# Kernel tuning notes

Hardware: AMD Instinct MI355X
Metric: run time of the kernel (lower is better)

## Reference

```python
import jax, jax.numpy as jnp
import numpy as np

N_HEAD, D_HEAD, D_MODEL = 16, 64, 1024
QLEN, MEMLEN, BSZ = 1024, 1024, 2
KLEN = QLEN + MEMLEN  # rlen == klen
LN_EPS = 1e-5
NEG = -1e30


def _rel_shift(x):
    # x: [qlen, rlen, bsz, n_head] -> Transformer-XL relative shift
    q, r, b, n = x.shape
    zp = jnp.zeros((q, 1, b, n), x.dtype)
    xp = jnp.concatenate([zp, x], axis=1).reshape(r + 1, q, b, n)
    return xp[1:].reshape(q, r, b, n)


def _layer_norm(x, gamma, beta):
    mu = jnp.mean(x, axis=-1, keepdims=True)
    var = jnp.mean((x - mu) ** 2, axis=-1, keepdims=True)
    return (x - mu) * jax.lax.rsqrt(var + LN_EPS) * gamma + beta


def setup_inputs() -> dict:
    key = jax.random.key(0)
    ks = jax.random.split(key, 8)
    w = jax.random.normal(ks[0], (QLEN, BSZ, D_MODEL), jnp.float32)
    r = jax.random.normal(ks[1], (KLEN, D_MODEL), jnp.float32)
    r_w_bias = jax.random.normal(ks[2], (N_HEAD, D_HEAD), jnp.float32) * 0.02
    r_r_bias = jax.random.normal(ks[3], (N_HEAD, D_HEAD), jnp.float32) * 0.02
    mems = jax.random.normal(ks[4], (MEMLEN, BSZ, D_MODEL), jnp.float32)
    W_qkv = jax.random.normal(ks[5], (D_MODEL, 3 * N_HEAD * D_HEAD), jnp.float32) * 0.02
    W_r = jax.random.normal(ks[6], (D_MODEL, N_HEAD * D_HEAD), jnp.float32) * 0.02
    W_o = jax.random.normal(ks[7], (N_HEAD * D_HEAD, D_MODEL), jnp.float32) * 0.02
    ln_gamma = jnp.ones((D_MODEL,), jnp.float32)
    ln_beta = jnp.zeros((D_MODEL,), jnp.float32)
    # causal mask with memory: key j visible to query i iff j <= i + MEMLEN (True = keep)
    attn_mask = jnp.arange(KLEN)[None, :] <= (jnp.arange(QLEN)[:, None] + MEMLEN)
    return {"w": w, "r": r, "r_w_bias": r_w_bias, "r_r_bias": r_r_bias,
            "mems": mems, "attn_mask": attn_mask, "W_qkv": W_qkv, "W_r": W_r,
            "W_o": W_o, "ln_gamma": ln_gamma, "ln_beta": ln_beta}


def reference(w, r, r_w_bias, r_r_bias, mems, attn_mask, W_qkv, W_r, W_o, ln_gamma, ln_beta):
    qlen, bsz = w.shape[0], w.shape[1]
    scale = 1.0 / (D_HEAD ** 0.5)
    cat = jnp.concatenate([mems, w], axis=0)            # [klen, b, d_model]
    klen = cat.shape[0]
    w_heads = cat @ W_qkv                                # [klen, b, 3*H*D]
    r_head_k = (r @ W_r).reshape(-1, N_HEAD, D_HEAD)     # [rlen, H, D]
    w_head_q, w_head_k, w_head_v = jnp.split(w_heads, 3, axis=-1)
    w_head_q = w_head_q[-qlen:].reshape(qlen, bsz, N_HEAD, D_HEAD)
    w_head_k = w_head_k.reshape(klen, bsz, N_HEAD, D_HEAD)
    w_head_v = w_head_v.reshape(klen, bsz, N_HEAD, D_HEAD)
    AC = jnp.einsum('ibnd,jbnd->ijbn', w_head_q + r_w_bias, w_head_k)
    BD = jnp.einsum('ibnd,jnd->ijbn', w_head_q + r_r_bias, r_head_k)
    BD = _rel_shift(BD)
    attn_score = (AC + BD) * scale                       # [q, k, b, n]
    attn_score = jnp.where(attn_mask[:, :, None, None], attn_score, NEG)
    attn_prob = jax.nn.softmax(attn_score, axis=1)
    attn_vec = jnp.einsum('ijbn,jbnd->ibnd', attn_prob, w_head_v)
    attn_vec = attn_vec.reshape(qlen, bsz, N_HEAD * D_HEAD)
    attn_out = attn_vec @ W_o                            # [q, b, d_model]
    return _layer_norm(w + attn_out, ln_gamma, ln_beta)
```

## Files before the change

### kernel.cpp

```cpp
#include <hip/hip_runtime.h>
#include <hip/hip_bf16.h>

#define NHEAD 16
#define DHEAD 64
#define DMODEL 1024
#define QLEN 1024
#define MEMLEN 1024
#define BSZ 2
#define KLEN 2048
#define LN_EPS 1e-5f

typedef __hip_bfloat16 bf16;
typedef __attribute__((ext_vector_type(8))) short short8;
typedef __attribute__((ext_vector_type(4))) float f32x4;

__device__ __forceinline__ float b2f(bf16 x) { return __bfloat162float(x); }
__device__ __forceinline__ bf16 f2b(float x) { return __float2bfloat16(x); }
__device__ __forceinline__ short f2bs(float f) {
    bf16 h = __float2bfloat16(f);
    return *reinterpret_cast<short*>(&h);
}
__device__ __forceinline__ float s2f(short s) {
    bf16 h = *reinterpret_cast<bf16*>(&s);
    return __bfloat162float(h);
}

#define MFMA16(a, b, c) __builtin_amdgcn_mfma_f32_16x16x32_bf16(a, b, c, 0, 0, 0)

#define AS1 __attribute__((address_space(1)))
#define AS3 __attribute__((address_space(3)))
__device__ __forceinline__ void gld16(const bf16* g, bf16* l) {
    __builtin_amdgcn_global_load_lds((const AS1 void*)(uintptr_t)g,
                                     (AS3 void*)(uint32_t)(uintptr_t)l, 16, 0, 0);
}

__global__ __launch_bounds__(256)
void prep(const float* __restrict__ mems, const float* __restrict__ w,
          const float* __restrict__ r, const float* __restrict__ Wqkv,
          const float* __restrict__ Wr, const float* __restrict__ Wo,
          bf16* __restrict__ Abf, bf16* __restrict__ rbf,
          bf16* __restrict__ Wqkvt, bf16* __restrict__ Wrt,
          bf16* __restrict__ Wot) {
    __shared__ bf16 T[64][65];
    const int id = blockIdx.x;
    const int t = threadIdx.x;
    if (id < 6144) {
        const float* src;
        bf16* dst;
        int off;
        if (id < 2048)      { src = mems; dst = Abf;                       off = id; }
        else if (id < 4096) { src = w;    dst = Abf + (size_t)2048 * 1024; off = id - 2048; }
        else                { src = r;    dst = rbf;                       off = id - 4096; }
        int i = off * 256 + t;
        const float4 v = reinterpret_cast<const float4*>(src)[i];
        bf16 o[4] = {f2b(v.x), f2b(v.y), f2b(v.z), f2b(v.w)};
        reinterpret_cast<ulong1*>(dst)[i] = *reinterpret_cast<ulong1*>(o);
        return;
    }
    int tid2 = id - 6144;
    const float* in;
    bf16* out;
    int N, tn, tile;
    if (tid2 < 768)       { in = Wqkv; out = Wqkvt; N = 3072; tn = 48; tile = tid2; }
    else if (tid2 < 1024) { in = Wr;   out = Wrt;   N = 1024; tn = 16; tile = tid2 - 768; }
    else                  { in = Wo;   out = Wot;   N = 1024; tn = 16; tile = tid2 - 1024; }
    const int K = 1024;
    const int n0 = (tile % tn) * 64, k0 = (tile / tn) * 64;
    #pragma unroll
    for (int e = 0; e < 16; e++) {
        int flat = e * 256 + t;
        int kl = flat >> 6, nl = flat & 63;
        T[kl][nl] = f2b(in[(size_t)(k0 + kl) * N + n0 + nl]);
    }
    __syncthreads();
    #pragma unroll
    for (int e = 0; e < 16; e++) {
        int flat = e * 256 + t;
        int nl = flat >> 6, kl = flat & 63;
        out[(size_t)(n0 + nl) * K + k0 + kl] = T[kl][nl];
    }
}

__global__ __launch_bounds__(256)
void gemm_mfma(const bf16* __restrict__ A, const bf16* __restrict__ Bt,
               const bf16* __restrict__ A2, const bf16* __restrict__ B2,
               int M, int N, int K, int mode,
               const float* __restrict__ rwb, const float* __restrict__ rrb,
               bf16* __restrict__ Qw, bf16* __restrict__ Qr,
               bf16* __restrict__ Kb, bf16* __restrict__ Vt,
               bf16* __restrict__ Cb, float* __restrict__ Cf) {
    const int bm = blockIdx.x * 128, bn = blockIdx.y * 128;
    int sub = 0;
    const bf16* Ap = A;
    const bf16* Bp = Bt;
    if (mode == 0 && bm < 2048 && bn < 1024) { sub = 1; Ap = A2; Bp = B2; }
    __shared__ bf16 As[128 * 32];
    __shared__ bf16 Bs[128 * 32];
    const int t = threadIdx.x;
    const int w = t >> 6, lane = t & 63, quad = lane >> 4, l16 = lane & 15;
    const int wm = (w >> 1) * 64, wn = (w & 1) * 64;
    const int lrow = lane >> 2, lcol = (lane & 3) * 8;

    f32x4 acc[4][4];
    #pragma unroll
    for (int mt = 0; mt < 4; mt++)
        #pragma unroll
        for (int nt = 0; nt < 4; nt++) acc[mt][nt] = (f32x4){0.f, 0.f, 0.f, 0.f};

    for (int k0 = 0; k0 < K; k0 += 32) {
        #pragma unroll
        for (int e = 0; e < 2; e++) {
            int ch = w + 4 * e;
            int row = ch * 16 + lrow;
            gld16(Ap + (size_t)(bm + row) * K + k0 + lcol, As + ch * 512);
            gld16(Bp + (size_t)(bn + row) * K + k0 + lcol, Bs + ch * 512);
        }
        __syncthreads();
        short8 af[4], bfr[4];
        #pragma unroll
        for (int mt = 0; mt < 4; mt++)
            af[mt] = *reinterpret_cast<short8*>(&As[(wm + 16 * mt + l16) * 32 + quad * 8]);
        #pragma unroll
        for (int nt = 0; nt < 4; nt++)
            bfr[nt] = *reinterpret_cast<short8*>(&Bs[(wn + 16 * nt + l16) * 32 + quad * 8]);
        #pragma unroll
        for (int mt = 0; mt < 4; mt++)
            #pragma unroll
            for (int nt = 0; nt < 4; nt++)
                acc[mt][nt] = MFMA16(af[mt], bfr[nt], acc[mt][nt]);
        __syncthreads();
    }

    #pragma unroll
    for (int mt = 0; mt < 4; mt++)
        #pragma unroll
        for (int nt = 0; nt < 4; nt++)
            #pragma unroll
            for (int r = 0; r < 4; r++) {
                int m = bm + wm + 16 * mt + quad * 4 + r;
                int c = bn + wn + 16 * nt + l16;
                float v = acc[mt][nt][r];
                if (sub) {
                    Cb[(size_t)m * 1024 + c] = f2b(v);
                } else if (mode == 0) {
                    int seg = c >> 10, cc = c & 1023;
                    if (seg == 0) {
                        if (m >= 2048) {
                            size_t o = (size_t)(m - 2048) * 1024 + cc;
                            Qw[o] = f2b(v + rwb[cc]);
                            Qr[o] = f2b(v + rrb[cc]);
                        }
                    } else if (seg == 1) {
                        Kb[(size_t)m * 1024 + cc] = f2b(v);
                    } else {
                        Vt[((size_t)cc * 2 + (m & 1)) * 2048 + (m >> 1)] = f2b(v);
                    }
                } else {
                    Cf[(size_t)m * N + c] = v;
                }
            }
}

__global__ __launch_bounds__(256, 3)
void attn_mfma(const bf16* __restrict__ Qw, const bf16* __restrict__ Qr,
               const bf16* __restrict__ Kb, const bf16* __restrict__ Vt,
               const bf16* __restrict__ Rk, float* __restrict__ Opart0,
               float* __restrict__ Opart1, float2* __restrict__ ML) {
    const int id = blockIdx.x;
    const int xcd = id & 7, local = id >> 3;
    const int quarter = local >> 5, idx = local & 31;
    const int a = idx >> 1, p = idx & 1;
    int i0, pidx, half;
    if (quarter < 2) { i0 = a;      pidx = p;     half = quarter; }
    else             { i0 = 15 - a; pidx = 2 + p; half = quarter - 2; }
    const int pair = xcd * 4 + pidx;
    const int b = pair & 1, n = pair >> 1;
    const int I0 = i0 * 64;
    const int T = i0 + 17;
    const int h0 = (T + 1) >> 1;
    const int t_beg = half ? h0 : 0;
    const int t_end = half ? T : h0;

    const int tid = threadIdx.x;
    const int w = tid >> 6, lane = tid & 63;
    const int quad = lane >> 4, l16 = lane & 15;
    const int qbase = I0 + 16 * w;
    const int ln8 = lane >> 3;
    const int cs = (lane & 7) ^ (ln8 & 7);
    const int q0 = (quad ^ (l16 & 7)) * 8;
    const int q1 = q0 ^ 32;

    __shared__ bf16 Ks[64 * 64];
    __shared__ bf16 Vs[64 * 64];
    __shared__ bf16 Rs[2][64 * 64];
    __shared__ short WlB_s[4][16 * 80];
    __shared__ short Pb_s[4][16 * 72];
    short* WlB = WlB_s[w];
    short* Pb = Pb_s[w];

    short8 aqw[2], aqr[2];
    {
        const bf16* qp = Qw + ((size_t)(qbase + l16) * 2 + b) * 1024 + n * 64 + quad * 8;
        aqw[0] = *reinterpret_cast<const short8*>(qp);
        aqw[1] = *reinterpret_cast<const short8*>(qp + 32);
        const bf16* qp2 = Qr + ((size_t)(qbase + l16) * 2 + b) * 1024 + n * 64 + quad * 8;
        aqr[0] = *reinterpret_cast<const short8*>(qp2);
        aqr[1] = *reinterpret_cast<const short8*>(qp2 + 32);
    }

    f32x4 O[4];
    #pragma unroll
    for (int d = 0; d < 4; d++) O[d] = (f32x4){0.f, 0.f, 0.f, 0.f};
    float m_run = -1e30f;
    float pl[4] = {0.f, 0.f, 0.f, 0.f};

    const int koff = b * 1024 + n * 64 + cs * 8;
    const size_t voff = (size_t)n * 262144 + b * 2048 + cs * 8;
    const int rcol = n * 64 + cs * 8;
    const int rbl = 48 - 16 * w;
    const int RB = 960 - I0;

    auto stageKV = [&](int tt) {
        const int J0 = tt * 64;
        #pragma unroll
        for (int e = 0; e < 2; e++) {
            int ch = w + 4 * e;
            int krow = J0 + ch * 8 + ln8;
            gld16(Kb + (size_t)krow * 2048 + koff, Ks + ch * 512);
            int dl = ch * 8 + ln8;
            gld16(Vt + (size_t)dl * 4096 + voff + J0, Vs + ch * 512);
        }
    };
    auto stageR = [&](int u) {
        bf16* rd = Rs[u & 1];
        #pragma unroll
        for (int e = 0; e < 2; e++) {
            int ch = w + 4 * e;
            int rrow = min(RB + u * 64 + ch * 8 + ln8, 2047);
            gld16(Rk + (size_t)rrow * 1024 + rcol, rd + ch * 512);
        }
    };

    stageR(t_beg);

    for (int tt = t_beg; tt < t_end; tt++) {
        stageKV(tt);
        stageR(tt + 1);
        __syncthreads();

        const bf16* R0 = Rs[tt & 1];
        const bf16* R1 = Rs[(tt + 1) & 1];
        const int J0 = tt * 64;

        #pragma unroll
        for (int s = 0; s < 5; s++) {
            int rb2 = rbl + 16 * s;
            const bf16* Rb = (rb2 & 64) ? R1 : R0;
            int rh = (rb2 & 63) + l16;
            short8 b0 = *reinterpret_cast<const short8*>(&Rb[rh * 64 + q0]);
            short8 b1 = *reinterpret_cast<const short8*>(&Rb[rh * 64 + q1]);
            f32x4 acc = (f32x4){0.f, 0.f, 0.f, 0.f};
            __builtin_amdgcn_s_setprio(1);
            acc = MFMA16(aqr[0], b0, acc);
            acc = MFMA16(aqr[1], b1, acc);
            __builtin_amdgcn_s_setprio(0);
            #pragma unroll
            for (int r = 0; r < 4; r++)
                WlB[(quad * 4 + r) * 80 + 16 * s + l16] = f2bs(acc[r]);
        }

        float sv[4][4];
        #pragma unroll
        for (int n16 = 0; n16 < 4; n16++) {
            int kr = 16 * n16 + l16;
            short8 k0 = *reinterpret_cast<const short8*>(&Ks[kr * 64 + q0]);
            short8 k1 = *reinterpret_cast<const short8*>(&Ks[kr * 64 + q1]);
            f32x4 acc = (f32x4){0.f, 0.f, 0.f, 0.f};
            __builtin_amdgcn_s_setprio(1);
            acc = MFMA16(aqw[0], k0, acc);
            acc = MFMA16(aqw[1], k1, acc);
            __builtin_amdgcn_s_setprio(0);
            #pragma unroll
            for (int r = 0; r < 4; r++) {
                int row = quad * 4 + r, col = 16 * n16 + l16;
                float s = (acc[r] + s2f(WlB[row * 80 + col - row + 15])) * 0.125f;
                if (J0 + col > qbase + row + MEMLEN) s = -1e30f;
                sv[n16][r] = s;
            }
        }

        float mx = sv[0][0];
        #pragma unroll
        for (int n16 = 0; n16 < 4; n16++)
            #pragma unroll
            for (int r = 0; r < 4; r++) mx = fmaxf(mx, sv[n16][r]);
        #pragma unroll
        for (int msk = 1; msk < 16; msk <<= 1) mx = fmaxf(mx, __shfl_xor(mx, msk));
        if (mx > m_run + 8.f) {
            const float alpha = __expf(m_run - mx);
            m_run = mx;
            #pragma unroll
            for (int r = 0; r < 4; r++) pl[r] *= alpha;
            #pragma unroll
            for (int d = 0; d < 4; d++)
                #pragma unroll
                for (int r = 0; r < 4; r++) O[d][r] *= alpha;
        }
        #pragma unroll
        for (int n16 = 0; n16 < 4; n16++)
            #pragma unroll
            for (int r = 0; r < 4; r++) sv[n16][r] = __expf(sv[n16][r] - m_run);
        #pragma unroll
        for (int r = 0; r < 4; r++)
            pl[r] += sv[0][r] + sv[1][r] + sv[2][r] + sv[3][r];

        #pragma unroll
        for (int n16 = 0; n16 < 4; n16++)
            #pragma unroll
            for (int r = 0; r < 4; r++)
                Pb[(quad * 4 + r) * 72 + 16 * n16 + l16] = f2bs(sv[n16][r]);
        short8 ap0 = *reinterpret_cast<short8*>(&Pb[l16 * 72 + quad * 8]);
        short8 ap1 = *reinterpret_cast<short8*>(&Pb[l16 * 72 + 32 + quad * 8]);

        __builtin_amdgcn_s_setprio(1);
        #pragma unroll
        for (int ds = 0; ds < 4; ds++) {
            int dr = 16 * ds + l16;
            short8 v0 = *reinterpret_cast<const short8*>(&Vs[dr * 64 + q0]);
            short8 v1 = *reinterpret_cast<const short8*>(&Vs[dr * 64 + q1]);
            O[ds] = MFMA16(ap0, v0, O[ds]);
            O[ds] = MFMA16(ap1, v1, O[ds]);
        }
        __builtin_amdgcn_s_setprio(0);

        __syncthreads();
    }

    float lr[4];
    #pragma unroll
    for (int r = 0; r < 4; r++) {
        float s = pl[r];
        #pragma unroll
        for (int msk = 1; msk < 16; msk <<= 1) s += __shfl_xor(s, msk);
        lr[r] = s;
    }
    if (l16 == 0) {
        #pragma unroll
        for (int r = 0; r < 4; r++) {
            int q = qbase + quad * 4 + r;
            ML[(size_t)half * 32768 + (q * 2 + b) * 16 + n] =
                make_float2(m_run, lr[r]);
        }
    }
    float* Od = half ? Opart1 : Opart0;
    #pragma unroll
    for (int ds = 0; ds < 4; ds++)
        #pragma unroll
        for (int r = 0; r < 4; r++) {
            int q = qbase + quad * 4 + r;
            Od[((size_t)q * 2 + b) * 1024 + n * 64 + 16 * ds + l16] =
                O[ds][r] / lr[r];
        }
}

__global__ __launch_bounds__(256)
void attn_combine(const float* __restrict__ O0, const float* __restrict__ O1,
                  const float2* __restrict__ ML, bf16* __restrict__ AVbf) {
    const int row = blockIdx.x;
    const int t = threadIdx.x;
    const int n = t >> 4;
    const float2 a0 = ML[row * 16 + n];
    const float2 a1 = ML[32768 + row * 16 + n];
    const float m = fmaxf(a0.x, a1.x);
    float w0 = a0.y * __expf(a0.x - m);
    float w1 = a1.y * __expf(a1.x - m);
    const float inv = 1.f / (w0 + w1);
    w0 *= inv; w1 *= inv;
    const f32x4 p0 = reinterpret_cast<const f32x4*>(O0)[row * 256 + t];
    const f32x4 p1 = reinterpret_cast<const f32x4*>(O1)[row * 256 + t];
    short o[4];
    #pragma unroll
    for (int j = 0; j < 4; j++) o[j] = f2bs(p0[j] * w0 + p1[j] * w1);
    reinterpret_cast<ulong1*>(AVbf)[row * 256 + t] = *reinterpret_cast<ulong1*>(o);
}

__global__ __launch_bounds__(256)
void ln_res(const float* __restrict__ ao, const float* __restrict__ w,
            const float* __restrict__ gamma, const float* __restrict__ beta,
            float* __restrict__ out) {
    const int m = blockIdx.x;
    const int t = threadIdx.x;
    __shared__ float red[256];
    float x[4];
    #pragma unroll
    for (int e = 0; e < 4; e++) {
        int c = e * 256 + t;
        x[e] = ao[(size_t)m * DMODEL + c] + w[(size_t)m * DMODEL + c];
    }
    float s = x[0] + x[1] + x[2] + x[3];
    red[t] = s;
    __syncthreads();
    #pragma unroll
    for (int off = 128; off; off >>= 1) {
        if (t < off) red[t] += red[t + off];
        __syncthreads();
    }
    const float mu = red[0] * (1.f / 1024.f);
    __syncthreads();
    float s2 = 0.f;
    #pragma unroll
    for (int e = 0; e < 4; e++) { float dx = x[e] - mu; s2 += dx * dx; }
    red[t] = s2;
    __syncthreads();
    #pragma unroll
    for (int off = 128; off; off >>= 1) {
        if (t < off) red[t] += red[t + off];
        __syncthreads();
    }
    const float rstd = rsqrtf(red[0] * (1.f / 1024.f) + LN_EPS);
    #pragma unroll
    for (int e = 0; e < 4; e++) {
        int c = e * 256 + t;
        out[(size_t)m * DMODEL + c] = (x[e] - mu) * rstd * gamma[c] + beta[c];
    }
}

extern "C" void kernel_launch(void* const* d_in, const int* in_sizes, int n_in,
                              void* d_out, int out_size, void* d_ws, size_t ws_size,
                              hipStream_t stream) {
    const float* w        = (const float*)d_in[0];
    const float* r        = (const float*)d_in[1];
    const float* r_w_bias = (const float*)d_in[2];
    const float* r_r_bias = (const float*)d_in[3];
    const float* mems     = (const float*)d_in[4];
    const float* W_qkv    = (const float*)d_in[6];
    const float* W_r      = (const float*)d_in[7];
    const float* W_o      = (const float*)d_in[8];
    const float* gamma    = (const float*)d_in[9];
    const float* beta     = (const float*)d_in[10];
    float* out = (float*)d_out;

    bf16* Abf    = (bf16*)d_ws;
    bf16* Wqkvt  = Abf   + (size_t)4096 * 1024;
    bf16* Wrt    = Wqkvt + (size_t)3072 * 1024;
    bf16* Wot    = Wrt   + (size_t)1024 * 1024;
    bf16* rbf    = Wot   + (size_t)1024 * 1024;
    bf16* Qw     = rbf   + (size_t)2048 * 1024;
    bf16* Qr     = Qw    + (size_t)2048 * 1024;
    bf16* Kb     = Qr    + (size_t)2048 * 1024;
    bf16* Vt     = Kb    + (size_t)4096 * 1024;
    bf16* Rk     = Vt    + (size_t)2048 * 2048;
    bf16* AVbf   = Rk    + (size_t)2048 * 1024;
    float* attn_out = (float*)Abf;
    float* Opart0   = (float*)Abf;
    float* Opart1   = (float*)Wqkvt;
    float2* ML      = (float2*)rbf;

    dim3 b256(256);
    prep<<<dim3(7424), b256, 0, stream>>>(mems, w, r, W_qkv, W_r, W_o,
                                          Abf, rbf, Wqkvt, Wrt, Wot);
    gemm_mfma<<<dim3(32, 24), b256, 0, stream>>>(
        Abf, Wqkvt, rbf, Wrt, 4096, 3072, 1024, 0, r_w_bias, r_r_bias,
        Qw, Qr, Kb, Vt, Rk, nullptr);
    attn_mfma<<<dim3(1024), b256, 0, stream>>>(Qw, Qr, Kb, Vt, Rk,
                                               Opart0, Opart1, ML);
    attn_combine<<<dim3(2048), b256, 0, stream>>>(Opart0, Opart1, ML, AVbf);
    gemm_mfma<<<dim3(16, 8), b256, 0, stream>>>(
        AVbf, Wot, nullptr, nullptr, 2048, 1024, 1024, 2, nullptr, nullptr,
        nullptr, nullptr, nullptr, nullptr, nullptr, attn_out);
    ln_res<<<dim3(QLEN * BSZ), b256, 0, stream>>>(attn_out, w, gamma, beta, out);
}
```

Baseline: 262.6 us.

## Rebalance attention work into paired query-tile chunks with direct global fragment loads

Result: slower. 338.2 us (+28.8%).

```diff
diff --git a/kernel.cpp b/kernel.cpp
--- a/kernel.cpp
+++ b/kernel.cpp
@@ -161,206 +161,199 @@
             }
 }
 
-__global__ __launch_bounds__(256, 3)
+__global__ __launch_bounds__(256)
 void attn_mfma(const bf16* __restrict__ Qw, const bf16* __restrict__ Qr,
                const bf16* __restrict__ Kb, const bf16* __restrict__ Vt,
-               const bf16* __restrict__ Rk, float* __restrict__ Opart0,
-               float* __restrict__ Opart1, float2* __restrict__ ML) {
+               const bf16* __restrict__ Rk, float* __restrict__ O0g,
+               float* __restrict__ O1g, float2* __restrict__ ML) {
     const int id = blockIdx.x;
     const int xcd = id & 7, local = id >> 3;
-    const int quarter = local >> 5, idx = local & 31;
-    const int a = idx >> 1, p = idx & 1;
-    int i0, pidx, half;
-    if (quarter < 2) { i0 = a;      pidx = p;     half = quarter; }
-    else             { i0 = 15 - a; pidx = 2 + p; half = quarter - 2; }
+    const int pidx = local & 3;
+    const int couple = (local >> 2) & 7;
+    const int chunk = local >> 5;
     const int pair = xcd * 4 + pidx;
     const int b = pair & 1, n = pair >> 1;
-    const int I0 = i0 * 64;
-    const int T = i0 + 17;
-    const int h0 = (T + 1) >> 1;
-    const int t_beg = half ? h0 : 0;
-    const int t_end = half ? T : h0;
+    const int TA = couple + 17;
+    const int t_beg = (chunk == 0) ? 0 : (chunk == 1) ? 17 : 33;
+    const int t_end = (chunk == 0) ? 17 : (chunk == 1) ? 33 : 49;
+
+    int segs[2][4];
+    int nseg = 0;
+    {
+        int aend = min(t_end, TA);
+        if (t_beg < aend) {
+            segs[nseg][0] = couple; segs[nseg][1] = t_beg;
+            segs[nseg][2] = aend;   segs[nseg][3] = (t_beg == 0) ? 0 : 1;
+            nseg++;
+        }
+        int bbeg = max(t_beg, TA);
+        if (bbeg < t_end) {
+            segs[nseg][0] = 15 - couple; segs[nseg][1] = bbeg - TA;
+            segs[nseg][2] = t_end - TA;  segs[nseg][3] = (bbeg == TA) ? 0 : 1;
+            nseg++;
+        }
+    }
 
     const int tid = threadIdx.x;
     const int w = tid >> 6, lane = tid & 63;
     const int quad = lane >> 4, l16 = lane & 15;
-    const int qbase = I0 + 16 * w;
-    const int ln8 = lane >> 3;
-    const int cs = (lane & 7) ^ (ln8 & 7);
-    const int q0 = (quad ^ (l16 & 7)) * 8;
-    const int q1 = q0 ^ 32;
-
-    __shared__ bf16 Ks[64 * 64];
-    __shared__ bf16 Vs[64 * 64];
-    __shared__ bf16 Rs[2][64 * 64];
+    const int rbl = 48 - 16 * w;
+
     __shared__ short WlB_s[4][16 * 80];
     __shared__ short Pb_s[4][16 * 72];
     short* WlB = WlB_s[w];
     short* Pb = Pb_s[w];
 
-    short8 aqw[2], aqr[2];
-    {
-        const bf16* qp = Qw + ((size_t)(qbase + l16) * 2 + b) * 1024 + n * 64 + quad * 8;
-        aqw[0] = *reinterpret_cast<const short8*>(qp);
-        aqw[1] = *reinterpret_cast<const short8*>(qp + 32);
-        const bf16* qp2 = Qr + ((size_t)(qbase + l16) * 2 + b) * 1024 + n * 64 + quad * 8;
-        aqr[0] = *reinterpret_cast<const short8*>(qp2);
-        aqr[1] = *reinterpret_cast<const short8*>(qp2 + 32);
-    }
-
-    f32x4 O[4];
-    #pragma unroll
-    for (int d = 0; d < 4; d++) O[d] = (f32x4){0.f, 0.f, 0.f, 0.f};
-    float m_run = -1e30f;
-    float pl[4] = {0.f, 0.f, 0.f, 0.f};
-
-    const int koff = b * 1024 + n * 64 + cs * 8;
-    const size_t voff = (size_t)n * 262144 + b * 2048 + cs * 8;
-    const int rcol = n * 64 + cs * 8;
-    const int rbl = 48 - 16 * w;
-    const int RB = 960 - I0;
-
-    auto stageKV = [&](int tt) {
-        const int J0 = tt * 64;
-        #pragma unroll
-        for (int e = 0; e < 2; e++) {
-            int ch = w + 4 * e;
-            int krow = J0 + ch * 8 + ln8;
-            gld16(Kb + (size_t)krow * 2048 + koff, Ks + ch * 512);
-            int dl = ch * 8 + ln8;
-            gld16(Vt + (size_t)dl * 4096 + voff + J0, Vs + ch * 512);
-        }
-    };
-    auto stageR = [&](int u) {
-        bf16* rd = Rs[u & 1];
-        #pragma unroll
-        for (int e = 0; e < 2; e++) {
-            int ch = w + 4 * e;
-            int rrow = min(RB + u * 64 + ch * 8 + ln8, 2047);
-            gld16(Rk + (size_t)rrow * 1024 + rcol, rd + ch * 512);
-        }
-    };
-
-    stageR(t_beg);
-
-    for (int tt = t_beg; tt < t_end; tt++) {
-        stageKV(tt);
-        stageR(tt + 1);
-        __syncthreads();
-
-        const bf16* R0 = Rs[tt & 1];
-        const bf16* R1 = Rs[(tt + 1) & 1];
-        const int J0 = tt * 64;
-
-        #pragma unroll
-        for (int s = 0; s < 5; s++) {
-            int rb2 = rbl + 16 * s;
-            const bf16* Rb = (rb2 & 64) ? R1 : R0;
-            int rh = (rb2 & 63) + l16;
-            short8 b0 = *reinterpret_cast<const short8*>(&Rb[rh * 64 + q0]);
-            short8 b1 = *reinterpret_cast<const short8*>(&Rb[rh * 64 + q1]);
-            f32x4 acc = (f32x4){0.f, 0.f, 0.f, 0.f};
+    const int rcol = n * 64 + quad * 8;
+    const int kcol = b * 1024 + n * 64 + quad * 8;
+    const size_t vrow0 = ((size_t)(n * 64 + l16) * 2 + b) * 2048 + quad * 8;
+
+    for (int sg = 0; sg < nseg; sg++) {
+        const int i0 = segs[sg][0], jb = segs[sg][1], je = segs[sg][2], slot = segs[sg][3];
+        const int I0 = i0 * 64;
+        const int qbase = I0 + 16 * w;
+        const int RB = 960 - I0;
+
+        short8 aqw[2], aqr[2];
+        {
+            const bf16* qp = Qw + ((size_t)(qbase + l16) * 2 + b) * 1024 + n * 64 + quad * 8;
+            aqw[0] = *reinterpret_cast<const short8*>(qp);
+            aqw[1] = *reinterpret_cast<const short8*>(qp + 32);
+            const bf16* qp2 = Qr + ((size_t)(qbase + l16) * 2 + b) * 1024 + n * 64 + quad * 8;
+            aqr[0] = *reinterpret_cast<const short8*>(qp2);
+            aqr[1] = *reinterpret_cast<const short8*>(qp2 + 32);
+        }
+
+        f32x4 O[4];
+        #pragma unroll
+        for (int d = 0; d < 4; d++) O[d] = (f32x4){0.f, 0.f, 0.f, 0.f};
+        float m_run = -1e30f;
+        float pl[4] = {0.f, 0.f, 0.f, 0.f};
+
+        for (int j = jb; j < je; j++) {
+            const int J0 = j * 64;
+
+            const int RBJ = RB + J0 + rbl;
+            short8 rf0[5], rf1[5];
+            #pragma unroll
+            for (int s = 0; s < 5; s++) {
+                int rr = min(RBJ + 16 * s + l16, 2047);
+                const bf16* rp = Rk + (size_t)rr * 1024 + rcol;
+                rf0[s] = *reinterpret_cast<const short8*>(rp);
+                rf1[s] = *reinterpret_cast<const short8*>(rp + 32);
+            }
+            short8 kf0[4], kf1[4];
+            #pragma unroll
+            for (int n16 = 0; n16 < 4; n16++) {
+                const bf16* kp = Kb + (size_t)(J0 + 16 * n16 + l16) * 2048 + kcol;
+                kf0[n16] = *reinterpret_cast<const short8*>(kp);
+                kf1[n16] = *reinterpret_cast<const short8*>(kp + 32);
+            }
+
+            #pragma unroll
+            for (int s = 0; s < 5; s++) {
+                f32x4 acc = (f32x4){0.f, 0.f, 0.f, 0.f};
+                __builtin_amdgcn_s_setprio(1);
+                acc = MFMA16(aqr[0], rf0[s], acc);
+                acc = MFMA16(aqr[1], rf1[s], acc);
+                __builtin_amdgcn_s_setprio(0);
+                #pragma unroll
+                for (int r = 0; r < 4; r++)
+                    WlB[(quad * 4 + r) * 80 + 16 * s + l16] = f2bs(acc[r]);
+            }
+
+            short8 vf0[4], vf1[4];
+            #pragma unroll
+            for (int ds = 0; ds < 4; ds++) {
+                const bf16* vp = Vt + (vrow0 + (size_t)ds * 65536 + J0);
+                vf0[ds] = *reinterpret_cast<const short8*>(vp);
+                vf1[ds] = *reinterpret_cast<const short8*>(vp + 32);
+            }
+
+            float sv[4][4];
+            #pragma unroll
+            for (int n16 = 0; n16 < 4; n16++) {
+                f32x4 acc = (f32x4){0.f, 0.f, 0.f, 0.f};
+                __builtin_amdgcn_s_setprio(1);
+                acc = MFMA16(aqw[0], kf0[n16], acc);
+                acc = MFMA16(aqw[1], kf1[n16], acc);
+                __builtin_amdgcn_s_setprio(0);
+                #pragma unroll
+                for (int r = 0; r < 4; r++) {
+                    int row = quad * 4 + r, col = 16 * n16 + l16;
+                    float s = (acc[r] + s2f(WlB[row * 80 + col - row + 15])) * 0.125f;
+                    if (J0 + col > qbase + row + MEMLEN) s = -1e30f;
+                    sv[n16][r] = s;
+                }
+            }
+
+            float mx = sv[0][0];
+            #pragma unroll
+            for (int n16 = 0; n16 < 4; n16++)
+                #pragma unroll
+                for (int r = 0; r < 4; r++) mx = fmaxf(mx, sv[n16][r]);
+            #pragma unroll
+            for (int msk = 1; msk < 16; msk <<= 1) mx = fmaxf(mx, __shfl_xor(mx, msk));
+            if (mx > m_run + 8.f) {
+                const float alpha = __expf(m_run - mx);
+                m_run = mx;
+                #pragma unroll
+                for (int r = 0; r < 4; r++) pl[r] *= alpha;
+                #pragma unroll
+                for (int d = 0; d < 4; d++)
+                    #pragma unroll
+                    for (int r = 0; r < 4; r++) O[d][r] *= alpha;
+            }
+            #pragma unroll
+            for (int n16 = 0; n16 < 4; n16++)
+                #pragma unroll
+                for (int r = 0; r < 4; r++) sv[n16][r] = __expf(sv[n16][r] - m_run);
+            #pragma unroll
+            for (int r = 0; r < 4; r++)
+                pl[r] += sv[0][r] + sv[1][r] + sv[2][r] + sv[3][r];
+
+            #pragma unroll
+            for (int n16 = 0; n16 < 4; n16++)
+                #pragma unroll
+                for (int r = 0; r < 4; r++)
+                    Pb[(quad * 4 + r) * 72 + 16 * n16 + l16] = f2bs(sv[n16][r]);
+            short8 ap0 = *reinterpret_cast<short8*>(&Pb[l16 * 72 + quad * 8]);
+            short8 ap1 = *reinterpret_cast<short8*>(&Pb[l16 * 72 + 32 + quad * 8]);
+
             __builtin_amdgcn_s_setprio(1);
-            acc = MFMA16(aqr[0], b0, acc);
-            acc = MFMA16(aqr[1], b1, acc);
+            #pragma unroll
+            for (int ds = 0; ds < 4; ds++) {
+                O[ds] = MFMA16(ap0, vf0[ds], O[ds]);
+                O[ds] = MFMA16(ap1, vf1[ds], O[ds]);
+            }
             __builtin_amdgcn_s_setprio(0);
-            #pragma unroll
-            for (int r = 0; r < 4; r++)
-                WlB[(quad * 4 + r) * 80 + 16 * s + l16] = f2bs(acc[r]);
-        }
-
-        float sv[4][4];
-        #pragma unroll
-        for (int n16 = 0; n16 < 4; n16++) {
-            int kr = 16 * n16 + l16;
-            short8 k0 = *reinterpret_cast<const short8*>(&Ks[kr * 64 + q0]);
-            short8 k1 = *reinterpret_cast<const short8*>(&Ks[kr * 64 + q1]);
-            f32x4 acc = (f32x4){0.f, 0.f, 0.f, 0.f};
-            __builtin_amdgcn_s_setprio(1);
-            acc = MFMA16(aqw[0], k0, acc);
-            acc = MFMA16(aqw[1], k1, acc);
-            __builtin_amdgcn_s_setprio(0);
+        }
+
+        float lr[4];
+        #pragma unroll
+        for (int r = 0; r < 4; r++) {
+            float s = pl[r];
+            #pragma unroll
+            for (int msk = 1; msk < 16; msk <<= 1) s += __shfl_xor(s, msk);
+            lr[r] = s;
+        }
+        if (l16 == 0) {
             #pragma unroll
             for (int r = 0; r < 4; r++) {
-                int row = quad * 4 + r, col = 16 * n16 + l16;
-                float s = (acc[r] + s2f(WlB[row * 80 + col - row + 15])) * 0.125f;
-                if (J0 + col > qbase + row + MEMLEN) s = -1e30f;
-                sv[n16][r] = s;
-            }
-        }
-
-        float mx = sv[0][0];
-        #pragma unroll
-        for (int n16 = 0; n16 < 4; n16++)
-            #pragma unroll
-            for (int r = 0; r < 4; r++) mx = fmaxf(mx, sv[n16][r]);
-        #pragma unroll
-        for (int msk = 1; msk < 16; msk <<= 1) mx = fmaxf(mx, __shfl_xor(mx, msk));
-        if (mx > m_run + 8.f) {
-            const float alpha = __expf(m_run - mx);
-            m_run = mx;
-            #pragma unroll
-            for (int r = 0; r < 4; r++) pl[r] *= alpha;
-            #pragma unroll
-            for (int d = 0; d < 4; d++)
-                #pragma unroll
-                for (int r = 0; r < 4; r++) O[d][r] *= alpha;
-        }
-        #pragma unroll
-        for (int n16 = 0; n16 < 4; n16++)
-            #pragma unroll
-            for (int r = 0; r < 4; r++) sv[n16][r] = __expf(sv[n16][r] - m_run);
-        #pragma unroll
-        for (int r = 0; r < 4; r++)
-            pl[r] += sv[0][r] + sv[1][r] + sv[2][r] + sv[3][r];
-
-        #pragma unroll
-        for (int n16 = 0; n16 < 4; n16++)
-            #pragma unroll
-            for (int r = 0; r < 4; r++)
-                Pb[(quad * 4 + r) * 72 + 16 * n16 + l16] = f2bs(sv[n16][r]);
-        short8 ap0 = *reinterpret_cast<short8*>(&Pb[l16 * 72 + quad * 8]);
-        short8 ap1 = *reinterpret_cast<short8*>(&Pb[l16 * 72 + 32 + quad * 8]);
-
-        __builtin_amdgcn_s_setprio(1);
-        #pragma unroll
-        for (int ds = 0; ds < 4; ds++) {
-            int dr = 16 * ds + l16;
-            short8 v0 = *reinterpret_cast<const short8*>(&Vs[dr * 64 + q0]);
-            short8 v1 = *reinterpret_cast<const short8*>(&Vs[dr * 64 + q1]);
-            O[ds] = MFMA16(ap0, v0, O[ds]);
-            O[ds] = MFMA16(ap1, v1, O[ds]);
-        }
-        __builtin_amdgcn_s_setprio(0);
-
-        __syncthreads();
-    }
-
-    float lr[4];
-    #pragma unroll
-    for (int r = 0; r < 4; r++) {
-        float s = pl[r];
-        #pragma unroll
-        for (int msk = 1; msk < 16; msk <<= 1) s += __shfl_xor(s, msk);
-        lr[r] = s;
-    }
-    if (l16 == 0) {
-        #pragma unroll
-        for (int r = 0; r < 4; r++) {
-            int q = qbase + quad * 4 + r;
-            ML[(size_t)half * 32768 + (q * 2 + b) * 16 + n] =
-                make_float2(m_run, lr[r]);
-        }
-    }
-    float* Od = half ? Opart1 : Opart0;
-    #pragma unroll
-    for (int ds = 0; ds < 4; ds++)
-        #pragma unroll
-        for (int r = 0; r < 4; r++) {
-            int q = qbase + quad * 4 + r;
-            Od[((size_t)q * 2 + b) * 1024 + n * 64 + 16 * ds + l16] =
-                O[ds][r] / lr[r];
-        }
+                int q = qbase + quad * 4 + r;
+                ML[(size_t)slot * 32768 + (q * 2 + b) * 16 + n] =
+                    make_float2(m_run, lr[r]);
+            }
+        }
+        float* Od = slot ? O1g : O0g;
+        #pragma unroll
+        for (int ds = 0; ds < 4; ds++)
+            #pragma unroll
+            for (int r = 0; r < 4; r++) {
+                int q = qbase + quad * 4 + r;
+                Od[((size_t)q * 2 + b) * 1024 + n * 64 + 16 * ds + l16] = O[ds][r];
+            }
+    }
 }
 
 __global__ __launch_bounds__(256)
@@ -369,18 +362,25 @@
     const int row = blockIdx.x;
     const int t = threadIdx.x;
     const int n = t >> 4;
+    const int i0 = row >> 7;
     const float2 a0 = ML[row * 16 + n];
-    const float2 a1 = ML[32768 + row * 16 + n];
-    const float m = fmaxf(a0.x, a1.x);
-    float w0 = a0.y * __expf(a0.x - m);
-    float w1 = a1.y * __expf(a1.x - m);
-    const float inv = 1.f / (w0 + w1);
-    w0 *= inv; w1 *= inv;
     const f32x4 p0 = reinterpret_cast<const f32x4*>(O0)[row * 256 + t];
-    const f32x4 p1 = reinterpret_cast<const f32x4*>(O1)[row * 256 + t];
     short o[4];
-    #pragma unroll
-    for (int j = 0; j < 4; j++) o[j] = f2bs(p0[j] * w0 + p1[j] * w1);
+    if (i0 != 0) {
+        const float2 a1 = ML[32768 + row * 16 + n];
+        const float m = fmaxf(a0.x, a1.x);
+        const float e0 = __expf(a0.x - m);
+        const float e1 = __expf(a1.x - m);
+        const float inv = 1.f / (a0.y * e0 + a1.y * e1);
+        const f32x4 p1 = reinterpret_cast<const f32x4*>(O1)[row * 256 + t];
+        #pragma unroll
+        for (int jj = 0; jj < 4; jj++)
+            o[jj] = f2bs((p0[jj] * e0 + p1[jj] * e1) * inv);
+    } else {
+        const float inv = 1.f / a0.y;
+        #pragma unroll
+        for (int jj = 0; jj < 4; jj++) o[jj] = f2bs(p0[jj] * inv);
+    }
     reinterpret_cast<ulong1*>(AVbf)[row * 256 + t] = *reinterpret_cast<ulong1*>(o);
 }
 
@@ -462,8 +462,8 @@
     gemm_mfma<<<dim3(32, 24), b256, 0, stream>>>(
         Abf, Wqkvt, rbf, Wrt, 4096, 3072, 1024, 0, r_w_bias, r_r_bias,
         Qw, Qr, Kb, Vt, Rk, nullptr);
-    attn_mfma<<<dim3(1024), b256, 0, stream>>>(Qw, Qr, Kb, Vt, Rk,
-                                               Opart0, Opart1, ML);
+    attn_mfma<<<dim3(768), b256, 0, stream>>>(Qw, Qr, Kb, Vt, Rk,
+                                              Opart0, Opart1, ML);
     attn_combine<<<dim3(2048), b256, 0, stream>>>(Opart0, Opart1, ML, AVbf);
     gemm_mfma<<<dim3(16, 8), b256, 0, stream>>>(
         AVbf, Wot, nullptr, nullptr, 2048, 1024, 1024, 2, nullptr, nullptr,
```
